# Optimization experiments

Measured on AMD Instinct MI355X. Metric: run time of the kernel, lower is better.

The kernel has to match this reference:

```python
import jax, jax.numpy as jnp
import numpy as np

B, N, D, E, K = 4, 4096, 2048, 128, 8


def setup_inputs() -> dict:
    key = jax.random.key(0)
    kx, kw, kb = jax.random.split(key, 3)
    x = jax.random.normal(kx, (B, N, D), dtype=jnp.float32)
    # nn.Linear(input_dim, num_experts): weight [E, D], bias [E]
    bound = 1.0 / np.sqrt(D)
    W = jax.random.uniform(kw, (E, D), dtype=jnp.float32, minval=-bound, maxval=bound)
    b = jax.random.uniform(kb, (E,), dtype=jnp.float32, minval=-bound, maxval=bound)
    return {"x": x, "W": W, "b": b}


def reference(x, W, b):
    # gate logits: [B, N, E]
    gate_logits = jnp.einsum("bnd,ed->bne", x, W) + b
    # top-k over experts
    topk_values, topk_indices = jax.lax.top_k(gate_logits, K)  # [B,N,K]
    topk_gates = jax.nn.softmax(topk_values, axis=-1)          # [B,N,K]
    # scatter normalized gates back into dense [B,N,E]
    onehot = jax.nn.one_hot(topk_indices, E, dtype=topk_gates.dtype)  # [B,N,K,E]
    full_gates = jnp.einsum("bnke,bnk->bne", onehot, topk_gates)
    return full_gates, topk_indices
```

## Files before the change

### kernel.cpp

```cpp
#include <hip/hip_runtime.h>
#include <cfloat>

#define TOKENS 16384
#define DDIM   2048
#define NEXP   128
#define KTOP   8
#define MB     64
#define CH     64
#define NCH    (DDIM / CH)
#define NTHR   512

typedef float    f32x4 __attribute__((ext_vector_type(4)));
typedef _Float16 f16x8 __attribute__((ext_vector_type(8)));

#define WFRAG_N (8 * NCH * 2 * 64)

__device__ __forceinline__ unsigned short f16bits(float f) {
    _Float16 h = (_Float16)f;
    return __builtin_bit_cast(unsigned short, h);
}
__device__ __forceinline__ float f16tof(unsigned short u) {
    return (float)__builtin_bit_cast(_Float16, u);
}

__global__ __launch_bounds__(256, 1) void wfrag_kernel(
    const float* __restrict__ W, uint4* __restrict__ wf)
{
    int id   = blockIdx.x * 256 + threadIdx.x;
    int lane = id & 63;
    int ks   = (id >> 6) & 1;
    int c    = (id >> 7) & (NCH - 1);
    int eb   = id >> 12;
    int e    = eb * 16 + (lane & 15);
    int k0   = c * CH + ks * 32 + (lane >> 4) * 8;
    const float* src = W + (size_t)e * DDIM + k0;
    unsigned hw[4], mw[4];
#pragma unroll
    for (int p = 0; p < 4; ++p) {
        float f0 = src[2 * p], f1 = src[2 * p + 1];
        unsigned short h0 = f16bits(f0), h1 = f16bits(f1);
        unsigned short m0 = f16bits((f0 - f16tof(h0)) * 4096.0f);
        unsigned short m1 = f16bits((f1 - f16tof(h1)) * 4096.0f);
        hw[p] = (unsigned)h0 | ((unsigned)h1 << 16);
        mw[p] = (unsigned)m0 | ((unsigned)m1 << 16);
    }
    wf[id]           = make_uint4(hw[0], hw[1], hw[2], hw[3]);
    wf[WFRAG_N + id] = make_uint4(mw[0], mw[1], mw[2], mw[3]);
}

__device__ __forceinline__ void insert8(float (&vals)[8], int (&idxs)[8], float v, int e) {
    bool c[8];
#pragma unroll
    for (int p = 0; p < 8; ++p) c[p] = v > vals[p];
#pragma unroll
    for (int p = 7; p >= 1; --p) {
        vals[p] = c[p] ? (c[p - 1] ? vals[p - 1] : v) : vals[p];
        idxs[p] = c[p] ? (c[p - 1] ? idxs[p - 1] : e) : idxs[p];
    }
    vals[0] = c[0] ? v : vals[0];
    idxs[0] = c[0] ? e : idxs[0];
}

__device__ __forceinline__ void chunk_barrier() {
    asm volatile("s_waitcnt lgkmcnt(0)" ::: "memory");
    __builtin_amdgcn_sched_barrier(0);
    __builtin_amdgcn_s_barrier();
    __builtin_amdgcn_sched_barrier(0);
}

__global__ __launch_bounds__(NTHR, 1) void router_kernel(
    const float* __restrict__ x, const uint4* __restrict__ wf,
    const float* __restrict__ b, float* __restrict__ out_gates,
    float* __restrict__ out_idx)
{
    __shared__ __align__(16) char smem[52224];
    float* lg  = (float*)smem;
    float* plv = (float*)(smem + 33792);
    int*   pli = (int*)(smem + 43008);

    const int tid  = threadIdx.x;
    const int lane = tid & 63;
    const int wid  = tid >> 6;
    const int tok0 = blockIdx.x * MB;

    const uint4* WFH = wf;
    const uint4* WFM = wf + WFRAG_N;

    f32x4 acc1[4], acc2[4];
#pragma unroll
    for (int mf = 0; mf < 4; ++mf) {
        acc1[mf] = (f32x4){0.f, 0.f, 0.f, 0.f};
        acc2[mf] = (f32x4){0.f, 0.f, 0.f, 0.f};
    }

    const float4* x4 = (const float4*)x;
    const int xr0 = tid >> 4, xr1 = 32 + (tid >> 4), xq = tid & 15;
    const size_t xoff0 = (size_t)(tok0 + xr0) * (DDIM / 4) + xq;
    const size_t xoff1 = (size_t)(tok0 + xr1) * (DDIM / 4) + xq;
    const int xb0 = xr0 * 128 + (((xq >> 1) ^ (xr0 & 7)) << 4) + (xq & 1) * 8;
    const int xb1 = xr1 * 128 + (((xq >> 1) ^ (xr1 & 7)) << 4) + (xq & 1) * 8;

    float4 S0[2], S1[2], S2[2], S3[2];
    uint4  wA[4], wB[4];

    auto loadX = [&](int c, float4 (&S)[2]) {
        S[0] = x4[xoff0 + (size_t)c * 16];
        S[1] = x4[xoff1 + (size_t)c * 16];
    };
    auto loadW = [&](int c, uint4 (&wreg)[4]) {
#pragma unroll
        for (int ks = 0; ks < 2; ++ks) {
            int idx = ((wid * NCH + c) * 2 + ks) * 64 + lane;
            wreg[ks]     = WFH[idx];
            wreg[2 + ks] = WFM[idx];
        }
    };
    auto convertX = [&](const float4 (&sx)[2], char* ldsDst) {
#pragma unroll
        for (int r = 0; r < 2; ++r) {
            const float4 v = sx[r];
            unsigned short h0 = f16bits(v.x), h1 = f16bits(v.y);
            unsigned short h2 = f16bits(v.z), h3 = f16bits(v.w);
            unsigned short m0 = f16bits((v.x - f16tof(h0)) * 4096.0f);
            unsigned short m1 = f16bits((v.y - f16tof(h1)) * 4096.0f);
            unsigned short m2 = f16bits((v.z - f16tof(h2)) * 4096.0f);
            unsigned short m3 = f16bits((v.w - f16tof(h3)) * 4096.0f);
            uint2 hv = make_uint2((unsigned)h0 | ((unsigned)h1 << 16),
                                  (unsigned)h2 | ((unsigned)h3 << 16));
            uint2 mv = make_uint2((unsigned)m0 | ((unsigned)m1 << 16),
                                  (unsigned)m2 | ((unsigned)m3 << 16));
            const int byteoff = r ? xb1 : xb0;
            *(uint2*)(ldsDst + byteoff)         = hv;
            *(uint2*)(ldsDst + 16384 + byteoff) = mv;
        }
    };

    auto step = [&](int c, float4 (&Sload)[2], float4 (&Scvt)[2],
                    uint4 (&wCur)[4], uint4 (&wNext)[4],
                    char* bufCur, char* bufNext) {
        if (c + 4 < NCH) loadX(c + 4, Sload);
        if (c + 1 < NCH) loadW(c + 1, wNext);

#pragma unroll
        for (int ks = 0; ks < 2; ++ks) {
            f16x8 ah[4], am[4];
#pragma unroll
            for (int mf = 0; mf < 4; ++mf) {
                int row = 16 * mf + (lane & 15);
                int byteoff = row * 128 +
                    ((((ks << 2) | (lane >> 4)) ^ (row & 7)) << 4);
                ah[mf] = *(const f16x8*)(bufCur + byteoff);
                am[mf] = *(const f16x8*)(bufCur + 16384 + byteoff);
            }
            f16x8 wh = __builtin_bit_cast(f16x8, wCur[ks]);
            f16x8 wm = __builtin_bit_cast(f16x8, wCur[2 + ks]);
#pragma unroll
            for (int mf = 0; mf < 4; ++mf) {
                acc1[mf] = __builtin_amdgcn_mfma_f32_16x16x32_f16(
                    ah[mf], wh, acc1[mf], 0, 0, 0);
                acc2[mf] = __builtin_amdgcn_mfma_f32_16x16x32_f16(
                    ah[mf], wm, acc2[mf], 0, 0, 0);
                acc2[mf] = __builtin_amdgcn_mfma_f32_16x16x32_f16(
                    am[mf], wh, acc2[mf], 0, 0, 0);
            }
        }

        if (c + 1 < NCH) convertX(Scvt, bufNext);
        chunk_barrier();
    };

    loadX(0, S0);
    loadX(1, S1);
    loadW(0, wA);
    loadX(2, S2);
    loadX(3, S3);
    convertX(S0, smem);
    chunk_barrier();

    char* buf0 = smem;
    char* buf1 = smem + 8192;
    for (int cc = 0; cc < NCH; cc += 4) {
        step(cc,     S0, S1, wA, wB, buf0, buf1);
        step(cc + 1, S1, S2, wB, wA, buf1, buf0);
        step(cc + 2, S2, S3, wA, wB, buf0, buf1);
        step(cc + 3, S3, S0, wB, wA, buf1, buf0);
    }

    const float bb = b[wid * 16 + (lane & 15)];
#pragma unroll
    for (int mf = 0; mf < 4; ++mf)
#pragma unroll
        for (int r = 0; r < 4; ++r) {
            int t = 16 * mf + (lane >> 4) * 4 + r;
            int e = wid * 16 + (lane & 15);
            lg[t * 132 + e] =
                fmaf(acc2[mf][r], 0.000244140625f, acc1[mf][r]) + bb;
        }
    __syncthreads();

    if (tid < 256) {
        int tt = tid >> 2, p = tid & 3;
        float vals[8]; int idxs[8];
#pragma unroll
        for (int k = 0; k < 8; ++k) { vals[k] = -FLT_MAX; idxs[k] = 0; }
        const float* row = &lg[tt * 132 + p * 32];
        for (int q = 0; q < 32; ++q)
            insert8(vals, idxs, row[q], p * 32 + q);
#pragma unroll
        for (int k = 0; k < 8; ++k) {
            plv[tid * 9 + k] = vals[k];
            pli[tid * 9 + k] = idxs[k];
        }
    }
    __syncthreads();

    float g[8]; int fidx[8];
    const bool active = (tid < MB);
    if (active) {
        float vals[8]; int idxs[8];
#pragma unroll
        for (int k = 0; k < 8; ++k) { vals[k] = -FLT_MAX; idxs[k] = 0; }
        for (int p = 0; p < 4; ++p) {
#pragma unroll
            for (int k = 0; k < 8; ++k)
                insert8(vals, idxs, plv[(tid * 4 + p) * 9 + k], pli[(tid * 4 + p) * 9 + k]);
        }
        float mx = vals[0];
        float s = 0.0f;
#pragma unroll
        for (int k = 0; k < 8; ++k) { g[k] = __expf(vals[k] - mx); s += g[k]; }
        float inv = 1.0f / s;
#pragma unroll
        for (int k = 0; k < 8; ++k) { g[k] *= inv; fidx[k] = idxs[k]; }
#pragma unroll
        for (int k = 0; k < 8; ++k)
            out_idx[(size_t)(tok0 + tid) * KTOP + k] = (float)idxs[k];
    }
    for (int f = tid; f < MB * 132; f += NTHR) lg[f] = 0.0f;
    __syncthreads();

    if (active) {
#pragma unroll
        for (int k = 0; k < 8; ++k) lg[tid * 132 + fidx[k]] = g[k];
    }
    __syncthreads();

    for (int f = tid; f < MB * (NEXP / 4); f += NTHR) {
        int m = f >> 5, e4 = f & 31;
        float4 v = *(const float4*)&lg[m * 132 + e4 * 4];
        ((float4*)out_gates)[(size_t)(tok0 + m) * (NEXP / 4) + e4] = v;
    }
}

extern "C" void kernel_launch(void* const* d_in, const int* in_sizes, int n_in,
                              void* d_out, int out_size, void* d_ws, size_t ws_size,
                              hipStream_t stream) {
    const float* x = (const float*)d_in[0];
    const float* W = (const float*)d_in[1];
    const float* b = (const float*)d_in[2];

    float* out_gates = (float*)d_out;
    float* out_idx   = out_gates + (size_t)TOKENS * NEXP;

    uint4* wf = (uint4*)d_ws;

    wfrag_kernel<<<dim3(WFRAG_N / 256), dim3(256), 0, stream>>>(W, wf);
    router_kernel<<<dim3(TOKENS / MB), dim3(NTHR), 0, stream>>>(x, wf, b, out_gates, out_idx);
}
```

Baseline: 53.86 us.

## Double K-chunk width to 128 and shorten x prefetch pipeline to two stages

Doubles the per-chunk K depth from 64 to 128, halving the number of chunk barriers and doubling the MFMA work per synchronisation. The LDS tiles grow to 256-byte rows with a 16-way XOR swizzle, and shared memory grows to 64 KiB. The x prefetch depth drops from four register stages to two, each holding twice the data. The W fragment prep now uses vectorised float4 loads. The shallower prefetch distance could expose more global load latency, and the larger register and LDS footprint may raise pressure.

```diff
diff --git a/kernel.cpp b/kernel.cpp
--- a/kernel.cpp
+++ b/kernel.cpp
@@ -6,14 +6,14 @@
 #define NEXP   128
 #define KTOP   8
 #define MB     64
-#define CH     64
+#define CH     128
 #define NCH    (DDIM / CH)
 #define NTHR   512
 
 typedef float    f32x4 __attribute__((ext_vector_type(4)));
 typedef _Float16 f16x8 __attribute__((ext_vector_type(8)));
 
-#define WFRAG_N (8 * NCH * 2 * 64)
+#define WFRAG_N (8 * 64 * 64)
 
 __device__ __forceinline__ unsigned short f16bits(float f) {
     _Float16 h = (_Float16)f;
@@ -29,18 +29,19 @@
     int id   = blockIdx.x * 256 + threadIdx.x;
     int lane = id & 63;
     int ks   = (id >> 6) & 1;
-    int c    = (id >> 7) & (NCH - 1);
+    int c    = (id >> 7) & 31;
     int eb   = id >> 12;
     int e    = eb * 16 + (lane & 15);
-    int k0   = c * CH + ks * 32 + (lane >> 4) * 8;
-    const float* src = W + (size_t)e * DDIM + k0;
+    int k0   = c * 64 + ks * 32 + (lane >> 4) * 8;
+    const float4* src = (const float4*)(W + (size_t)e * DDIM + k0);
+    float4 a = src[0], bq = src[1];
+    float v[8] = {a.x, a.y, a.z, a.w, bq.x, bq.y, bq.z, bq.w};
     unsigned hw[4], mw[4];
 #pragma unroll
     for (int p = 0; p < 4; ++p) {
-        float f0 = src[2 * p], f1 = src[2 * p + 1];
-        unsigned short h0 = f16bits(f0), h1 = f16bits(f1);
-        unsigned short m0 = f16bits((f0 - f16tof(h0)) * 4096.0f);
-        unsigned short m1 = f16bits((f1 - f16tof(h1)) * 4096.0f);
+        unsigned short h0 = f16bits(v[2 * p]), h1 = f16bits(v[2 * p + 1]);
+        unsigned short m0 = f16bits((v[2 * p]     - f16tof(h0)) * 4096.0f);
+        unsigned short m1 = f16bits((v[2 * p + 1] - f16tof(h1)) * 4096.0f);
         hw[p] = (unsigned)h0 | ((unsigned)h1 << 16);
         mw[p] = (unsigned)m0 | ((unsigned)m1 << 16);
     }
@@ -73,7 +74,7 @@
     const float* __restrict__ b, float* __restrict__ out_gates,
     float* __restrict__ out_idx)
 {
-    __shared__ __align__(16) char smem[52224];
+    __shared__ __align__(16) char smem[65536];
     float* lg  = (float*)smem;
     float* plv = (float*)(smem + 33792);
     int*   pli = (int*)(smem + 43008);
@@ -97,63 +98,67 @@
     const int xr0 = tid >> 4, xr1 = 32 + (tid >> 4), xq = tid & 15;
     const size_t xoff0 = (size_t)(tok0 + xr0) * (DDIM / 4) + xq;
     const size_t xoff1 = (size_t)(tok0 + xr1) * (DDIM / 4) + xq;
-    const int xb0 = xr0 * 128 + (((xq >> 1) ^ (xr0 & 7)) << 4) + (xq & 1) * 8;
-    const int xb1 = xr1 * 128 + (((xq >> 1) ^ (xr1 & 7)) << 4) + (xq & 1) * 8;
-
-    float4 S0[2], S1[2], S2[2], S3[2];
-    uint4  wA[4], wB[4];
-
-    auto loadX = [&](int c, float4 (&S)[2]) {
-        S[0] = x4[xoff0 + (size_t)c * 16];
-        S[1] = x4[xoff1 + (size_t)c * 16];
-    };
-    auto loadW = [&](int c, uint4 (&wreg)[4]) {
-#pragma unroll
-        for (int ks = 0; ks < 2; ++ks) {
-            int idx = ((wid * NCH + c) * 2 + ks) * 64 + lane;
+
+    float4 S0[4], S1[4];
+    uint4  wA[8], wB[8];
+
+    auto loadX = [&](int c, float4 (&S)[4]) {
+        const size_t o = (size_t)c * 32;
+        S[0] = x4[xoff0 + o];  S[1] = x4[xoff0 + o + 16];
+        S[2] = x4[xoff1 + o];  S[3] = x4[xoff1 + o + 16];
+    };
+    auto loadW = [&](int c, uint4 (&wreg)[8]) {
+#pragma unroll
+        for (int ks = 0; ks < 4; ++ks) {
+            int idx = (wid * 64 + c * 4 + ks) * 64 + lane;
             wreg[ks]     = WFH[idx];
-            wreg[2 + ks] = WFM[idx];
-        }
-    };
-    auto convertX = [&](const float4 (&sx)[2], char* ldsDst) {
-#pragma unroll
-        for (int r = 0; r < 2; ++r) {
-            const float4 v = sx[r];
-            unsigned short h0 = f16bits(v.x), h1 = f16bits(v.y);
-            unsigned short h2 = f16bits(v.z), h3 = f16bits(v.w);
-            unsigned short m0 = f16bits((v.x - f16tof(h0)) * 4096.0f);
-            unsigned short m1 = f16bits((v.y - f16tof(h1)) * 4096.0f);
-            unsigned short m2 = f16bits((v.z - f16tof(h2)) * 4096.0f);
-            unsigned short m3 = f16bits((v.w - f16tof(h3)) * 4096.0f);
-            uint2 hv = make_uint2((unsigned)h0 | ((unsigned)h1 << 16),
-                                  (unsigned)h2 | ((unsigned)h3 << 16));
-            uint2 mv = make_uint2((unsigned)m0 | ((unsigned)m1 << 16),
-                                  (unsigned)m2 | ((unsigned)m3 << 16));
-            const int byteoff = r ? xb1 : xb0;
-            *(uint2*)(ldsDst + byteoff)         = hv;
-            *(uint2*)(ldsDst + 16384 + byteoff) = mv;
-        }
-    };
-
-    auto step = [&](int c, float4 (&Sload)[2], float4 (&Scvt)[2],
-                    uint4 (&wCur)[4], uint4 (&wNext)[4],
+            wreg[4 + ks] = WFM[idx];
+        }
+    };
+    auto convertX = [&](const float4 (&S)[4], char* hbase) {
+#pragma unroll
+        for (int r = 0; r < 2; ++r)
+#pragma unroll
+            for (int cc = 0; cc < 2; ++cc) {
+                const float4 v = S[r * 2 + cc];
+                const int row = r ? xr1 : xr0;
+                const int q   = xq + 16 * cc;
+                unsigned short h0 = f16bits(v.x), h1 = f16bits(v.y);
+                unsigned short h2 = f16bits(v.z), h3 = f16bits(v.w);
+                unsigned short m0 = f16bits((v.x - f16tof(h0)) * 4096.0f);
+                unsigned short m1 = f16bits((v.y - f16tof(h1)) * 4096.0f);
+                unsigned short m2 = f16bits((v.z - f16tof(h2)) * 4096.0f);
+                unsigned short m3 = f16bits((v.w - f16tof(h3)) * 4096.0f);
+                uint2 hv = make_uint2((unsigned)h0 | ((unsigned)h1 << 16),
+                                      (unsigned)h2 | ((unsigned)h3 << 16));
+                uint2 mv = make_uint2((unsigned)m0 | ((unsigned)m1 << 16),
+                                      (unsigned)m2 | ((unsigned)m3 << 16));
+                const int byteoff = row * 256 +
+                    (((q >> 1) ^ (row & 15)) << 4) + (q & 1) * 8;
+                *(uint2*)(hbase + byteoff)         = hv;
+                *(uint2*)(hbase + 32768 + byteoff) = mv;
+            }
+    };
+
+    auto step = [&](int c, float4 (&Sload)[4], float4 (&Scvt)[4],
+                    uint4 (&wCur)[8], uint4 (&wNext)[8],
                     char* bufCur, char* bufNext) {
-        if (c + 4 < NCH) loadX(c + 4, Sload);
+        if (c + 2 < NCH) loadX(c + 2, Sload);
         if (c + 1 < NCH) loadW(c + 1, wNext);
 
 #pragma unroll
-        for (int ks = 0; ks < 2; ++ks) {
+        for (int ks = 0; ks < 4; ++ks) {
             f16x8 ah[4], am[4];
 #pragma unroll
             for (int mf = 0; mf < 4; ++mf) {
                 int row = 16 * mf + (lane & 15);
-                int byteoff = row * 128 +
-                    ((((ks << 2) | (lane >> 4)) ^ (row & 7)) << 4);
+                int s16 = (ks * 4 + (lane >> 4)) ^ (row & 15);
+                int byteoff = row * 256 + (s16 << 4);
                 ah[mf] = *(const f16x8*)(bufCur + byteoff);
-                am[mf] = *(const f16x8*)(bufCur + 16384 + byteoff);
+                am[mf] = *(const f16x8*)(bufCur + 32768 + byteoff);
             }
             f16x8 wh = __builtin_bit_cast(f16x8, wCur[ks]);
-            f16x8 wm = __builtin_bit_cast(f16x8, wCur[2 + ks]);
+            f16x8 wm = __builtin_bit_cast(f16x8, wCur[4 + ks]);
 #pragma unroll
             for (int mf = 0; mf < 4; ++mf) {
                 acc1[mf] = __builtin_amdgcn_mfma_f32_16x16x32_f16(
@@ -172,18 +177,14 @@
     loadX(0, S0);
     loadX(1, S1);
     loadW(0, wA);
-    loadX(2, S2);
-    loadX(3, S3);
     convertX(S0, smem);
     chunk_barrier();
 
     char* buf0 = smem;
-    char* buf1 = smem + 8192;
-    for (int cc = 0; cc < NCH; cc += 4) {
+    char* buf1 = smem + 16384;
+    for (int cc = 0; cc < NCH; cc += 2) {
         step(cc,     S0, S1, wA, wB, buf0, buf1);
-        step(cc + 1, S1, S2, wB, wA, buf1, buf0);
-        step(cc + 2, S2, S3, wA, wB, buf0, buf1);
-        step(cc + 3, S3, S0, wB, wA, buf1, buf0);
+        step(cc + 1, S1, S0, wB, wA, buf1, buf0);
     }
 
     const float bb = b[wid * 16 + (lane & 15)];
```

Result: no change. 53.97 us (+0.2%).

## Fuse weight fp16 split conversion into router kernel, drop prep launch

Applied to the files above, without the earlier changes.

Removes the separate wfrag_kernel that pre-split W into fp16 hi/lo fragments and instead loads raw fp32 W rows directly, converting them to hi/lo fp16 in registers each chunk. This saves one kernel launch and the workspace round trip. In exchange, each of the 256 blocks redundantly converts the full W (16 values per lane per chunk) and reads twice as many bytes of W as fp32, adding VALU work and L2 traffic inside the MFMA loop.

```diff
diff --git a/kernel.cpp b/kernel.cpp
--- a/kernel.cpp
+++ b/kernel.cpp
@@ -13,39 +13,12 @@
 typedef float    f32x4 __attribute__((ext_vector_type(4)));
 typedef _Float16 f16x8 __attribute__((ext_vector_type(8)));
 
-#define WFRAG_N (8 * NCH * 2 * 64)
-
 __device__ __forceinline__ unsigned short f16bits(float f) {
     _Float16 h = (_Float16)f;
     return __builtin_bit_cast(unsigned short, h);
 }
 __device__ __forceinline__ float f16tof(unsigned short u) {
     return (float)__builtin_bit_cast(_Float16, u);
-}
-
-__global__ __launch_bounds__(256, 1) void wfrag_kernel(
-    const float* __restrict__ W, uint4* __restrict__ wf)
-{
-    int id   = blockIdx.x * 256 + threadIdx.x;
-    int lane = id & 63;
-    int ks   = (id >> 6) & 1;
-    int c    = (id >> 7) & (NCH - 1);
-    int eb   = id >> 12;
-    int e    = eb * 16 + (lane & 15);
-    int k0   = c * CH + ks * 32 + (lane >> 4) * 8;
-    const float* src = W + (size_t)e * DDIM + k0;
-    unsigned hw[4], mw[4];
-#pragma unroll
-    for (int p = 0; p < 4; ++p) {
-        float f0 = src[2 * p], f1 = src[2 * p + 1];
-        unsigned short h0 = f16bits(f0), h1 = f16bits(f1);
-        unsigned short m0 = f16bits((f0 - f16tof(h0)) * 4096.0f);
-        unsigned short m1 = f16bits((f1 - f16tof(h1)) * 4096.0f);
-        hw[p] = (unsigned)h0 | ((unsigned)h1 << 16);
-        mw[p] = (unsigned)m0 | ((unsigned)m1 << 16);
-    }
-    wf[id]           = make_uint4(hw[0], hw[1], hw[2], hw[3]);
-    wf[WFRAG_N + id] = make_uint4(mw[0], mw[1], mw[2], mw[3]);
 }
 
 __device__ __forceinline__ void insert8(float (&vals)[8], int (&idxs)[8], float v, int e) {
@@ -69,7 +42,7 @@
 }
 
 __global__ __launch_bounds__(NTHR, 1) void router_kernel(
-    const float* __restrict__ x, const uint4* __restrict__ wf,
+    const float* __restrict__ x, const float* __restrict__ W,
     const float* __restrict__ b, float* __restrict__ out_gates,
     float* __restrict__ out_idx)
 {
@@ -83,9 +56,6 @@
     const int wid  = tid >> 6;
     const int tok0 = blockIdx.x * MB;
 
-    const uint4* WFH = wf;
-    const uint4* WFM = wf + WFRAG_N;
-
     f32x4 acc1[4], acc2[4];
 #pragma unroll
     for (int mf = 0; mf < 4; ++mf) {
@@ -100,19 +70,28 @@
     const int xb0 = xr0 * 128 + (((xq >> 1) ^ (xr0 & 7)) << 4) + (xq & 1) * 8;
     const int xb1 = xr1 * 128 + (((xq >> 1) ^ (xr1 & 7)) << 4) + (xq & 1) * 8;
 
+    const float4* wb4 = (const float4*)(W + (size_t)(wid * 16 + (lane & 15)) * DDIM)
+                        + (lane >> 4) * 2;
+
     float4 S0[2], S1[2], S2[2], S3[2];
-    uint4  wA[4], wB[4];
+    float4 wrawA[4], wrawB[4];
 
     auto loadX = [&](int c, float4 (&S)[2]) {
         S[0] = x4[xoff0 + (size_t)c * 16];
         S[1] = x4[xoff1 + (size_t)c * 16];
     };
-    auto loadW = [&](int c, uint4 (&wreg)[4]) {
-#pragma unroll
-        for (int ks = 0; ks < 2; ++ks) {
-            int idx = ((wid * NCH + c) * 2 + ks) * 64 + lane;
-            wreg[ks]     = WFH[idx];
-            wreg[2 + ks] = WFM[idx];
+    auto loadWraw = [&](int c, float4 (&wr)[4]) {
+        wr[0] = wb4[c * 16];      wr[1] = wb4[c * 16 + 1];
+        wr[2] = wb4[c * 16 + 8];  wr[3] = wb4[c * 16 + 9];
+    };
+    auto convW = [&](const float4& a, const float4& bq, f16x8& wh, f16x8& wm) {
+        float v[8] = {a.x, a.y, a.z, a.w, bq.x, bq.y, bq.z, bq.w};
+#pragma unroll
+        for (int i = 0; i < 8; ++i) {
+            unsigned short hb = f16bits(v[i]);
+            unsigned short mb = f16bits((v[i] - f16tof(hb)) * 4096.0f);
+            wh[i] = __builtin_bit_cast(_Float16, hb);
+            wm[i] = __builtin_bit_cast(_Float16, mb);
         }
     };
     auto convertX = [&](const float4 (&sx)[2], char* ldsDst) {
@@ -136,10 +115,14 @@
     };
 
     auto step = [&](int c, float4 (&Sload)[2], float4 (&Scvt)[2],
-                    uint4 (&wCur)[4], uint4 (&wNext)[4],
+                    float4 (&wrCur)[4], float4 (&wrNext)[4],
                     char* bufCur, char* bufNext) {
         if (c + 4 < NCH) loadX(c + 4, Sload);
-        if (c + 1 < NCH) loadW(c + 1, wNext);
+        if (c + 1 < NCH) loadWraw(c + 1, wrNext);
+
+        f16x8 wh[2], wm[2];
+        convW(wrCur[0], wrCur[1], wh[0], wm[0]);
+        convW(wrCur[2], wrCur[3], wh[1], wm[1]);
 
 #pragma unroll
         for (int ks = 0; ks < 2; ++ks) {
@@ -152,16 +135,14 @@
                 ah[mf] = *(const f16x8*)(bufCur + byteoff);
                 am[mf] = *(const f16x8*)(bufCur + 16384 + byteoff);
             }
-            f16x8 wh = __builtin_bit_cast(f16x8, wCur[ks]);
-            f16x8 wm = __builtin_bit_cast(f16x8, wCur[2 + ks]);
 #pragma unroll
             for (int mf = 0; mf < 4; ++mf) {
                 acc1[mf] = __builtin_amdgcn_mfma_f32_16x16x32_f16(
-                    ah[mf], wh, acc1[mf], 0, 0, 0);
+                    ah[mf], wh[ks], acc1[mf], 0, 0, 0);
                 acc2[mf] = __builtin_amdgcn_mfma_f32_16x16x32_f16(
-                    ah[mf], wm, acc2[mf], 0, 0, 0);
+                    ah[mf], wm[ks], acc2[mf], 0, 0, 0);
                 acc2[mf] = __builtin_amdgcn_mfma_f32_16x16x32_f16(
-                    am[mf], wh, acc2[mf], 0, 0, 0);
+                    am[mf], wh[ks], acc2[mf], 0, 0, 0);
             }
         }
 
@@ -171,7 +152,7 @@
 
     loadX(0, S0);
     loadX(1, S1);
-    loadW(0, wA);
+    loadWraw(0, wrawA);
     loadX(2, S2);
     loadX(3, S3);
     convertX(S0, smem);
@@ -180,10 +161,10 @@
     char* buf0 = smem;
     char* buf1 = smem + 8192;
     for (int cc = 0; cc < NCH; cc += 4) {
-        step(cc,     S0, S1, wA, wB, buf0, buf1);
-        step(cc + 1, S1, S2, wB, wA, buf1, buf0);
-        step(cc + 2, S2, S3, wA, wB, buf0, buf1);
-        step(cc + 3, S3, S0, wB, wA, buf1, buf0);
+        step(cc,     S0, S1, wrawA, wrawB, buf0, buf1);
+        step(cc + 1, S1, S2, wrawB, wrawA, buf1, buf0);
+        step(cc + 2, S2, S3, wrawA, wrawB, buf0, buf1);
+        step(cc + 3, S3, S0, wrawB, wrawA, buf1, buf0);
     }
 
     const float bb = b[wid * 16 + (lane & 15)];
@@ -262,8 +243,6 @@
     float* out_gates = (float*)d_out;
     float* out_idx   = out_gates + (size_t)TOKENS * NEXP;
 
-    uint4* wf = (uint4*)d_ws;
-
-    wfrag_kernel<<<dim3(WFRAG_N / 256), dim3(256), 0, stream>>>(W, wf);
-    router_kernel<<<dim3(TOKENS / MB), dim3(NTHR), 0, stream>>>(x, wf, b, out_gates, out_idx);
-}
+    router_kernel<<<dim3(TOKENS / MB), dim3(NTHR), 0, stream>>>(
+        x, W, b, out_gates, out_idx);
+}
```

New measurement: 65.74 us. 1.22x slower.
